# Kernel tuning notes

Hardware: AMD Instinct MI355X
Metric: run time of the kernel (lower is better)

The kernel has to match this reference:

```python
import jax, jax.numpy as jnp
import numpy as np

F = 64    # input features
H = 3     # hidden units (hardcoded in the original module)
B = 2048  # batch
T = 512   # timesteps


def setup_inputs() -> dict:
    key = jax.random.key(0)
    ks = jax.random.split(key, 6)
    x = jax.random.normal(ks[0], (B, T, F), dtype=jnp.float32)
    # Keras LSTM kernels: kernel [F, 4H], recurrent_kernel [H, 4H], bias [4H]
    # glorot_uniform scale for kernel
    lim_k = float(np.sqrt(6.0 / (F + 4 * H)))
    W = jax.random.uniform(ks[1], (F, 4 * H), minval=-lim_k, maxval=lim_k, dtype=jnp.float32)
    lim_u = float(np.sqrt(6.0 / (H + 4 * H)))
    U = jax.random.uniform(ks[2], (H, 4 * H), minval=-lim_u, maxval=lim_u, dtype=jnp.float32)
    # Keras default LSTM bias: zeros with forget-gate bias = 1 (unit_forget_bias=True)
    b = jnp.zeros((4 * H,), dtype=jnp.float32).at[H:2 * H].set(1.0)
    lim_d = float(np.sqrt(6.0 / (H + 1)))
    Wd = jax.random.uniform(ks[3], (H, 1), minval=-lim_d, maxval=lim_d, dtype=jnp.float32)
    bd = 0.05 * jax.random.normal(ks[4], (1,), dtype=jnp.float32)  # truncated_normal init
    return {"x": x, "W": W, "U": U, "b": b, "Wd": Wd, "bd": bd}


def _lstm_last_h(x, W, U, b):
    # x: [B, T, F] -> scan over time; gate order in Keras: i, f, g(c), o
    Bsz = x.shape[0]
    h0 = jnp.zeros((Bsz, H), dtype=x.dtype)
    c0 = jnp.zeros((Bsz, H), dtype=x.dtype)

    def step(carry, xt):
        h, c = carry
        z = xt @ W + h @ U + b                     # [B, 4H]
        i = jax.nn.sigmoid(z[:, 0 * H:1 * H])
        f = jax.nn.sigmoid(z[:, 1 * H:2 * H])
        g = jnp.tanh(z[:, 2 * H:3 * H])
        o = jax.nn.sigmoid(z[:, 3 * H:4 * H])
        c_new = f * c + i * g
        h_new = o * jnp.tanh(c_new)
        return (h_new, c_new), None

    (hT, _), _ = jax.lax.scan(step, (h0, c0), jnp.swapaxes(x, 0, 1))  # [T, B, F]
    return hT  # [B, H]


def reference(x, W, U, b, Wd, bd):
    hT = _lstm_last_h(x, W, U, b)
    return jax.nn.sigmoid(hT @ Wd + bd)  # [B, 1]
```

## Files before the change

### kernel.cpp

```cpp
#include <hip/hip_runtime.h>
#include <hip/hip_bf16.h>
#include <cstdint>

#define B_SZ 2048
#define T_SZ 512
#define F_SZ 64
#define BPB  4
#define TCH  32
#define NCHK (T_SZ / TCH)
#define NBLK (B_SZ / BPB)
#define NTHR 256
#define ROWS (BPB * TCH)
#define MT   (ROWS / 16)
#define NPC  (ROWS * 16)
#define NSTG 128
#define PPT  (NPC / NSTG)
#define TSTR 84
#define ESTR 20

#define L2E 1.4426950408889634f

typedef __attribute__((ext_vector_type(8))) short short8;
typedef __attribute__((ext_vector_type(4))) float f32x4;

__device__ __forceinline__ float fast_rcp(float x) { return __builtin_amdgcn_rcpf(x); }
__device__ __forceinline__ float exp2h(float x)    { return __builtin_amdgcn_exp2f(x); }
__device__ __forceinline__ float sigm_s(float zs)  { return fast_rcp(1.0f + exp2h(zs)); }
__device__ __forceinline__ float sigm_n(float x)   { return sigm_s(x * (-L2E)); }

__device__ __forceinline__ unsigned short f2bf(float f) {
    __hip_bfloat16 h = (__hip_bfloat16)f;
    return *reinterpret_cast<unsigned short*>(&h);
}

template<int CTRL>
__device__ __forceinline__ float dppmv(float v) {
    return __int_as_float(__builtin_amdgcn_mov_dpp(__float_as_int(v), CTRL, 0xF, 0xF, true));
}
#define DPP_SHR6 0x116
#define DPP_SHR3 0x113
#define DPP_SHL3 0x103
#define DPP_NB6  0x156
#define DPP_NB7  0x157
#define DPP_NB8  0x158

__global__ __launch_bounds__(NTHR) void lstm_mfma(const float* __restrict__ x,
                                                  const float* __restrict__ W,
                                                  const float* __restrict__ U,
                                                  const float* __restrict__ bias,
                                                  const float* __restrict__ Wd,
                                                  const float* __restrict__ bdp,
                                                  float* __restrict__ out) {
    __shared__ unsigned int xfrag[2][MT * 2 * 256];
    __shared__ float zbuf[2][(TCH + 4) * TSTR];

    const int tid = threadIdx.x;
    const int wv  = tid >> 6;
    const int ln  = tid & 63;
    const int b0  = blockIdx.x * BPB;

    const int n  = ln & 15;
    const int q  = n / 3;
    const float scq = (q == 2) ? (-2.0f * L2E) : (-L2E);

    short8 bfrag[2];
    #pragma unroll
    for (int kt = 0; kt < 2; ++kt) {
        short8 s;
        #pragma unroll
        for (int e = 0; e < 8; ++e) {
            const int hh = e >> 2, j = e & 3;
            const int kk = kt * 32 + hh * 16 + 4 * (ln >> 4) + j;
            const float w = (n < 12 && wv == 1) ? W[kk * 12 + n] * scq : 0.0f;
            s[e] = (short)f2bf(w);
        }
        bfrag[kt] = s;
    }
    const float bias_s = (n < 12) ? bias[n] * scq : 0.0f;

    const int e16 = ln >> 4;
    float u0 = 0.f, u1 = 0.f, u2 = 0.f, gA = 0.f, gB = 0.f;
    if (n < 12) {
        u0 = U[0 * 12 + n] * scq;
        u1 = U[1 * 12 + n] * scq;
        u2 = U[2 * 12 + n] * scq;
        if (q == 2) { gA = -4.0f * L2E; gB = 2.0f * L2E; }
        else        { gA = 1.0f;        gB = 0.0f;       }
    }
    float cs = 0.f, h0b = 0.f, h1b = 0.f, h2b = 0.f;

    auto comp = [&](float z4) {
        const float z  = fmaf(h0b, u0, fmaf(h1b, u1, fmaf(h2b, u2, z4)));
        const float r  = fast_rcp(1.0f + exp2h(z));
        const float gt = fmaf(gA, r, gB);
        const float iV = dppmv<DPP_SHR6>(gt);
        const float fV = dppmv<DPP_SHR3>(gt);
        const float oV = dppmv<DPP_SHL3>(gt);
        cs = fmaf(fV, cs, iV * gt);
        const float th = fmaf(2.0f, fast_rcp(1.0f + exp2h(cs)), -1.0f);
        const float h  = oV * th;
        h0b = dppmv<DPP_NB6>(h);
        h1b = dppmv<DPP_NB7>(h);
        h2b = dppmv<DPP_NB8>(h);
    };

    auto scan32 = [&](const float* zb) {
        const float* zp = zb + e16 * ESTR + n;
        float pf[4];
        #pragma unroll
        for (int i = 0; i < 4; ++i) pf[i] = zp[i * TSTR];
        __builtin_amdgcn_s_setprio(1);
        #pragma unroll 4
        for (int tt = 0; tt < TCH; ++tt) {
            const float z4 = pf[tt & 3];
            pf[tt & 3] = zp[(tt + 4) * TSTR];
            comp(z4);
        }
        __builtin_amdgcn_s_setprio(0);
    };

    float4 v[PPT];
    const int stid = tid - 128;
    auto stage_issue = [&](int ck) {
        const int t0 = ck * TCH;
        #pragma unroll
        for (int i = 0; i < PPT; ++i) {
            const int piece = i * NSTG + stid;
            const int row = piece >> 4, g = piece & 15;
            v[i] = *reinterpret_cast<const float4*>(
                x + ((size_t)(b0 + (row >> 5)) * T_SZ + (t0 + (row & 31))) * F_SZ + (g << 2));
        }
    };
    auto stage_write = [&](int buf) {
        #pragma unroll
        for (int i = 0; i < PPT; ++i) {
            const int piece = i * NSTG + stid;
            const int row = piece >> 4, g = piece & 15;
            const int u_off = ((row >> 4) * 2 + (g >> 3)) * 256
                            + (((row & 15) | ((g & 3) << 4)) << 2) + ((g >> 2) & 1) * 2;
            uint2 pk;
            pk.x = (unsigned)f2bf(v[i].x) | ((unsigned)f2bf(v[i].y) << 16);
            pk.y = (unsigned)f2bf(v[i].z) | ((unsigned)f2bf(v[i].w) << 16);
            *reinterpret_cast<uint2*>(&xfrag[buf][u_off]) = pk;
        }
    };

    auto mfma_chunk = [&](int cur) {
        #pragma unroll
        for (int mt = 0; mt < MT; ++mt) {
            f32x4 acc = { bias_s, bias_s, bias_s, bias_s };
            const short8 a0 = *reinterpret_cast<const short8*>(&xfrag[cur][(mt * 2 + 0) * 256 + (ln << 2)]);
            const short8 a1 = *reinterpret_cast<const short8*>(&xfrag[cur][(mt * 2 + 1) * 256 + (ln << 2)]);
            acc = __builtin_amdgcn_mfma_f32_16x16x32_bf16(a0, bfrag[0], acc, 0, 0, 0);
            acc = __builtin_amdgcn_mfma_f32_16x16x32_bf16(a1, bfrag[1], acc, 0, 0, 0);
            const int rbase = mt * 16 + 4 * (ln >> 4);
            #pragma unroll
            for (int r = 0; r < 4; ++r) {
                const int rr = rbase + r;
                zbuf[cur][(rr & 31) * TSTR + (rr >> 5) * ESTR + n] = acc[r];
            }
        }
    };

    if (wv >= 2) { stage_issue(0); stage_write(0); }
    __syncthreads();

    for (int k = 0; k < NCHK; ++k) {
        const int cur = k & 1;
        if (wv >= 2) {
            if (k + 1 < NCHK) { stage_issue(k + 1); stage_write(cur ^ 1); }
        } else if (wv == 1) {
            mfma_chunk(cur);
        } else if (k > 0) {
            scan32(zbuf[cur ^ 1]);
        }
        __syncthreads();
    }

    if (wv == 0) {
        scan32(zbuf[(NCHK - 1) & 1]);
        if (n == 0) {
            const float logit = bdp[0] + h0b * Wd[0] + h1b * Wd[1] + h2b * Wd[2];
            out[b0 + e16] = sigm_n(logit);
        }
    }
}

extern "C" void kernel_launch(void* const* d_in, const int* in_sizes, int n_in,
                              void* d_out, int out_size, void* d_ws, size_t ws_size,
                              hipStream_t stream) {
    (void)in_sizes; (void)n_in; (void)out_size; (void)d_ws; (void)ws_size;
    const float* x  = (const float*)d_in[0];
    const float* W  = (const float*)d_in[1];
    const float* U  = (const float*)d_in[2];
    const float* b  = (const float*)d_in[3];
    const float* Wd = (const float*)d_in[4];
    const float* bd = (const float*)d_in[5];
    float* out = (float*)d_out;

    lstm_mfma<<<NBLK, NTHR, 0, stream>>>(x, W, U, b, Wd, bd, out);
}
```

Baseline: 53.52 us.

## Use one batch row per block, load x directly in MFMA wave

```diff
diff --git a/kernel.cpp b/kernel.cpp
--- a/kernel.cpp
+++ b/kernel.cpp
@@ -5,18 +5,13 @@
 #define B_SZ 2048
 #define T_SZ 512
 #define F_SZ 64
-#define BPB  4
-#define TCH  32
+#define BPB  1
+#define TCH  128
 #define NCHK (T_SZ / TCH)
 #define NBLK (B_SZ / BPB)
-#define NTHR 256
-#define ROWS (BPB * TCH)
-#define MT   (ROWS / 16)
-#define NPC  (ROWS * 16)
-#define NSTG 128
-#define PPT  (NPC / NSTG)
-#define TSTR 84
-#define ESTR 20
+#define NTHR 128
+#define MT   (TCH / 16)
+#define ZSTR 17
 
 #define L2E 1.4426950408889634f
 
@@ -44,22 +39,23 @@
 #define DPP_NB7  0x157
 #define DPP_NB8  0x158
 
-__global__ __launch_bounds__(NTHR) void lstm_mfma(const float* __restrict__ x,
-                                                  const float* __restrict__ W,
-                                                  const float* __restrict__ U,
-                                                  const float* __restrict__ bias,
-                                                  const float* __restrict__ Wd,
-                                                  const float* __restrict__ bdp,
-                                                  float* __restrict__ out) {
-    __shared__ unsigned int xfrag[2][MT * 2 * 256];
-    __shared__ float zbuf[2][(TCH + 4) * TSTR];
+__global__ __launch_bounds__(NTHR, 4) void lstm_mfma(const float* __restrict__ x,
+                                                     const float* __restrict__ W,
+                                                     const float* __restrict__ U,
+                                                     const float* __restrict__ bias,
+                                                     const float* __restrict__ Wd,
+                                                     const float* __restrict__ bdp,
+                                                     float* __restrict__ out) {
+    __shared__ float zbuf[2][(TCH + 4) * ZSTR];
 
     const int tid = threadIdx.x;
     const int wv  = tid >> 6;
     const int ln  = tid & 63;
-    const int b0  = blockIdx.x * BPB;
+    const int lr  = ln & 15;
+    const int lg  = ln >> 4;
+    const size_t bb = blockIdx.x;
 
-    const int n  = ln & 15;
+    const int n  = lr;
     const int q  = n / 3;
     const float scq = (q == 2) ? (-2.0f * L2E) : (-L2E);
 
@@ -70,7 +66,7 @@
         #pragma unroll
         for (int e = 0; e < 8; ++e) {
             const int hh = e >> 2, j = e & 3;
-            const int kk = kt * 32 + hh * 16 + 4 * (ln >> 4) + j;
+            const int kk = kt * 32 + hh * 16 + 4 * lg + j;
             const float w = (n < 12 && wv == 1) ? W[kk * 12 + n] * scq : 0.0f;
             s[e] = (short)f2bf(w);
         }
@@ -78,7 +74,6 @@
     }
     const float bias_s = (n < 12) ? bias[n] * scq : 0.0f;
 
-    const int e16 = ln >> 4;
     float u0 = 0.f, u1 = 0.f, u2 = 0.f, gA = 0.f, gB = 0.f;
     if (n < 12) {
         u0 = U[0 * 12 + n] * scq;
@@ -104,84 +99,62 @@
         h2b = dppmv<DPP_NB8>(h);
     };
 
-    auto scan32 = [&](const float* zb) {
-        const float* zp = zb + e16 * ESTR + n;
+    auto scan128 = [&](const float* zb) {
+        const float* zp = zb + n;
         float pf[4];
         #pragma unroll
-        for (int i = 0; i < 4; ++i) pf[i] = zp[i * TSTR];
+        for (int i = 0; i < 4; ++i) pf[i] = zp[i * ZSTR];
         __builtin_amdgcn_s_setprio(1);
         #pragma unroll 4
         for (int tt = 0; tt < TCH; ++tt) {
             const float z4 = pf[tt & 3];
-            pf[tt & 3] = zp[(tt + 4) * TSTR];
+            pf[tt & 3] = zp[(tt + 4) * ZSTR];
             comp(z4);
         }
         __builtin_amdgcn_s_setprio(0);
     };
 
-    float4 v[PPT];
-    const int stid = tid - 128;
-    auto stage_issue = [&](int ck) {
-        const int t0 = ck * TCH;
-        #pragma unroll
-        for (int i = 0; i < PPT; ++i) {
-            const int piece = i * NSTG + stid;
-            const int row = piece >> 4, g = piece & 15;
-            v[i] = *reinterpret_cast<const float4*>(
-                x + ((size_t)(b0 + (row >> 5)) * T_SZ + (t0 + (row & 31))) * F_SZ + (g << 2));
-        }
-    };
-    auto stage_write = [&](int buf) {
-        #pragma unroll
-        for (int i = 0; i < PPT; ++i) {
-            const int piece = i * NSTG + stid;
-            const int row = piece >> 4, g = piece & 15;
-            const int u_off = ((row >> 4) * 2 + (g >> 3)) * 256
-                            + (((row & 15) | ((g & 3) << 4)) << 2) + ((g >> 2) & 1) * 2;
-            uint2 pk;
-            pk.x = (unsigned)f2bf(v[i].x) | ((unsigned)f2bf(v[i].y) << 16);
-            pk.y = (unsigned)f2bf(v[i].z) | ((unsigned)f2bf(v[i].w) << 16);
-            *reinterpret_cast<uint2*>(&xfrag[buf][u_off]) = pk;
-        }
-    };
-
-    auto mfma_chunk = [&](int cur) {
+    auto mfma_period = [&](int p) {
+        const int buf = p & 1;
+        const float* xb = x + ((size_t)bb * T_SZ + p * TCH) * F_SZ;
         #pragma unroll
         for (int mt = 0; mt < MT; ++mt) {
+            const float* xr = xb + (size_t)(mt * 16 + lr) * F_SZ + 4 * lg;
+            const float4 v00 = *reinterpret_cast<const float4*>(xr + 0);
+            const float4 v01 = *reinterpret_cast<const float4*>(xr + 16);
+            const float4 v10 = *reinterpret_cast<const float4*>(xr + 32);
+            const float4 v11 = *reinterpret_cast<const float4*>(xr + 48);
+            short8 a0, a1;
+            a0[0] = (short)f2bf(v00.x); a0[1] = (short)f2bf(v00.y);
+            a0[2] = (short)f2bf(v00.z); a0[3] = (short)f2bf(v00.w);
+            a0[4] = (short)f2bf(v01.x); a0[5] = (short)f2bf(v01.y);
+            a0[6] = (short)f2bf(v01.z); a0[7] = (short)f2bf(v01.w);
+            a1[0] = (short)f2bf(v10.x); a1[1] = (short)f2bf(v10.y);
+            a1[2] = (short)f2bf(v10.z); a1[3] = (short)f2bf(v10.w);
+            a1[4] = (short)f2bf(v11.x); a1[5] = (short)f2bf(v11.y);
+            a1[6] = (short)f2bf(v11.z); a1[7] = (short)f2bf(v11.w);
             f32x4 acc = { bias_s, bias_s, bias_s, bias_s };
-            const short8 a0 = *reinterpret_cast<const short8*>(&xfrag[cur][(mt * 2 + 0) * 256 + (ln << 2)]);
-            const short8 a1 = *reinterpret_cast<const short8*>(&xfrag[cur][(mt * 2 + 1) * 256 + (ln << 2)]);
             acc = __builtin_amdgcn_mfma_f32_16x16x32_bf16(a0, bfrag[0], acc, 0, 0, 0);
             acc = __builtin_amdgcn_mfma_f32_16x16x32_bf16(a1, bfrag[1], acc, 0, 0, 0);
-            const int rbase = mt * 16 + 4 * (ln >> 4);
             #pragma unroll
             for (int r = 0; r < 4; ++r) {
-                const int rr = rbase + r;
-                zbuf[cur][(rr & 31) * TSTR + (rr >> 5) * ESTR + n] = acc[r];
+                const int t = mt * 16 + 4 * lg + r;
+                zbuf[buf][t * ZSTR + lr] = acc[r];
             }
         }
     };
 
-    if (wv >= 2) { stage_issue(0); stage_write(0); }
-    __syncthreads();
-
-    for (int k = 0; k < NCHK; ++k) {
-        const int cur = k & 1;
-        if (wv >= 2) {
-            if (k + 1 < NCHK) { stage_issue(k + 1); stage_write(cur ^ 1); }
-        } else if (wv == 1) {
-            mfma_chunk(cur);
-        } else if (k > 0) {
-            scan32(zbuf[cur ^ 1]);
-        }
+    for (int p = 0; p < NCHK; ++p) {
+        if (wv == 1) mfma_period(p);
+        else if (p > 0) scan128(zbuf[(p - 1) & 1]);
         __syncthreads();
     }
 
     if (wv == 0) {
-        scan32(zbuf[(NCHK - 1) & 1]);
-        if (n == 0) {
+        scan128(zbuf[(NCHK - 1) & 1]);
+        if (ln == 0) {
             const float logit = bdp[0] + h0b * Wd[0] + h1b * Wd[1] + h2b * Wd[2];
-            out[b0 + e16] = sigm_n(logit);
+            out[bb] = sigm_n(logit);
         }
     }
 }
```

Result: slower. 69.68 us (+30.2%).

## Halve batch per block, lengthen chunks, single-buffer x with LDS flag handoff

Applied to the files above, without the earlier changes.

```diff
diff --git a/kernel.cpp b/kernel.cpp
--- a/kernel.cpp
+++ b/kernel.cpp
@@ -5,8 +5,8 @@
 #define B_SZ 2048
 #define T_SZ 512
 #define F_SZ 64
-#define BPB  4
-#define TCH  32
+#define BPB  2
+#define TCH  64
 #define NCHK (T_SZ / TCH)
 #define NBLK (B_SZ / BPB)
 #define NTHR 256
@@ -15,8 +15,8 @@
 #define NPC  (ROWS * 16)
 #define NSTG 128
 #define PPT  (NPC / NSTG)
-#define TSTR 84
-#define ESTR 20
+#define TSTR 33
+#define ESTR 16
 
 #define L2E 1.4426950408889634f
 
@@ -44,20 +44,33 @@
 #define DPP_NB7  0x157
 #define DPP_NB8  0x158
 
-__global__ __launch_bounds__(NTHR) void lstm_mfma(const float* __restrict__ x,
-                                                  const float* __restrict__ W,
-                                                  const float* __restrict__ U,
-                                                  const float* __restrict__ bias,
-                                                  const float* __restrict__ Wd,
-                                                  const float* __restrict__ bdp,
-                                                  float* __restrict__ out) {
-    __shared__ unsigned int xfrag[2][MT * 2 * 256];
+__device__ __forceinline__ void wait_flag(volatile int* f) {
+    if (!*f) { while (!*f) __builtin_amdgcn_s_sleep(8); }
+    asm volatile("s_waitcnt lgkmcnt(0)" ::: "memory");
+}
+__device__ __forceinline__ void set_flag(volatile int* f, int ln) {
+    asm volatile("s_waitcnt lgkmcnt(0)" ::: "memory");
+    if (ln == 0) *f = 1;
+}
+
+__global__ __launch_bounds__(NTHR, 4) void lstm_mfma(const float* __restrict__ x,
+                                                     const float* __restrict__ W,
+                                                     const float* __restrict__ U,
+                                                     const float* __restrict__ bias,
+                                                     const float* __restrict__ Wd,
+                                                     const float* __restrict__ bdp,
+                                                     float* __restrict__ out) {
+    __shared__ unsigned int xfrag[MT * 2 * 256];
     __shared__ float zbuf[2][(TCH + 4) * TSTR];
+    __shared__ int xwr2[NCHK], xwr3[NCHK], xrd[NCHK];
 
     const int tid = threadIdx.x;
     const int wv  = tid >> 6;
     const int ln  = tid & 63;
     const int b0  = blockIdx.x * BPB;
+
+    if (tid < NCHK) { xwr2[tid] = 0; xwr3[tid] = 0; xrd[tid] = 0; }
+    __syncthreads();
 
     const int n  = ln & 15;
     const int q  = n / 3;
@@ -78,7 +91,7 @@
     }
     const float bias_s = (n < 12) ? bias[n] * scq : 0.0f;
 
-    const int e16 = ln >> 4;
+    const int e16 = (ln >> 4) & 1;
     float u0 = 0.f, u1 = 0.f, u2 = 0.f, gA = 0.f, gB = 0.f;
     if (n < 12) {
         u0 = U[0 * 12 + n] * scq;
@@ -104,7 +117,7 @@
         h2b = dppmv<DPP_NB8>(h);
     };
 
-    auto scan32 = [&](const float* zb) {
+    auto scan64 = [&](const float* zb) {
         const float* zp = zb + e16 * ESTR + n;
         float pf[4];
         #pragma unroll
@@ -128,10 +141,10 @@
             const int piece = i * NSTG + stid;
             const int row = piece >> 4, g = piece & 15;
             v[i] = *reinterpret_cast<const float4*>(
-                x + ((size_t)(b0 + (row >> 5)) * T_SZ + (t0 + (row & 31))) * F_SZ + (g << 2));
-        }
-    };
-    auto stage_write = [&](int buf) {
+                x + ((size_t)(b0 + (row >> 6)) * T_SZ + (t0 + (row & 63))) * F_SZ + (g << 2));
+        }
+    };
+    auto stage_write = [&]() {
         #pragma unroll
         for (int i = 0; i < PPT; ++i) {
             const int piece = i * NSTG + stid;
@@ -141,45 +154,57 @@
             uint2 pk;
             pk.x = (unsigned)f2bf(v[i].x) | ((unsigned)f2bf(v[i].y) << 16);
             pk.y = (unsigned)f2bf(v[i].z) | ((unsigned)f2bf(v[i].w) << 16);
-            *reinterpret_cast<uint2*>(&xfrag[buf][u_off]) = pk;
-        }
-    };
-
-    auto mfma_chunk = [&](int cur) {
+            *reinterpret_cast<uint2*>(&xfrag[u_off]) = pk;
+        }
+    };
+
+    auto mfma_period = [&](int p) {
         #pragma unroll
         for (int mt = 0; mt < MT; ++mt) {
             f32x4 acc = { bias_s, bias_s, bias_s, bias_s };
-            const short8 a0 = *reinterpret_cast<const short8*>(&xfrag[cur][(mt * 2 + 0) * 256 + (ln << 2)]);
-            const short8 a1 = *reinterpret_cast<const short8*>(&xfrag[cur][(mt * 2 + 1) * 256 + (ln << 2)]);
+            const short8 a0 = *reinterpret_cast<const short8*>(&xfrag[(mt * 2 + 0) * 256 + (ln << 2)]);
+            const short8 a1 = *reinterpret_cast<const short8*>(&xfrag[(mt * 2 + 1) * 256 + (ln << 2)]);
             acc = __builtin_amdgcn_mfma_f32_16x16x32_bf16(a0, bfrag[0], acc, 0, 0, 0);
             acc = __builtin_amdgcn_mfma_f32_16x16x32_bf16(a1, bfrag[1], acc, 0, 0, 0);
             const int rbase = mt * 16 + 4 * (ln >> 4);
             #pragma unroll
             for (int r = 0; r < 4; ++r) {
                 const int rr = rbase + r;
-                zbuf[cur][(rr & 31) * TSTR + (rr >> 5) * ESTR + n] = acc[r];
+                zbuf[p & 1][(rr & 63) * TSTR + (rr >> 6) * ESTR + n] = acc[r];
             }
         }
     };
 
-    if (wv >= 2) { stage_issue(0); stage_write(0); }
+    if (wv >= 2) {
+        stage_issue(0);
+        stage_write();
+        set_flag((wv == 2) ? &xwr2[0] : &xwr3[0], ln);
+        stage_issue(1);
+    }
     __syncthreads();
 
-    for (int k = 0; k < NCHK; ++k) {
-        const int cur = k & 1;
+    for (int p = 0; p < NCHK; ++p) {
         if (wv >= 2) {
-            if (k + 1 < NCHK) { stage_issue(k + 1); stage_write(cur ^ 1); }
+            if (p + 1 < NCHK) {
+                wait_flag(&xrd[p]);
+                stage_write();
+                set_flag((wv == 2) ? &xwr2[p + 1] : &xwr3[p + 1], ln);
+                if (p + 2 < NCHK) stage_issue(p + 2);
+            }
         } else if (wv == 1) {
-            mfma_chunk(cur);
-        } else if (k > 0) {
-            scan32(zbuf[cur ^ 1]);
+            wait_flag(&xwr2[p]);
+            wait_flag(&xwr3[p]);
+            mfma_period(p);
+            set_flag(&xrd[p], ln);
+        } else if (p > 0) {
+            scan64(zbuf[(p - 1) & 1]);
         }
         __syncthreads();
     }
 
     if (wv == 0) {
-        scan32(zbuf[(NCHK - 1) & 1]);
-        if (n == 0) {
+        scan64(zbuf[(NCHK - 1) & 1]);
+        if (n == 0 && ln < 32) {
             const float logit = bdp[0] + h0b * Wd[0] + h1b * Wd[1] + h2b * Wd[2];
             out[b0 + e16] = sigm_n(logit);
         }
```

New measurement: 107.3 us. 2x slower.
